# Kernel optimization log

Measured on AMD Instinct MI355X. Metric: run time of the kernel, lower is better.

Reference implementation:

```python
import jax, jax.numpy as jnp
import numpy as np

# ---- model dims (match init_kwargs) ----
BATCH, SEQ, DM = 2, 256, 768
EXPAND, HD, NST = 2, 64, 64
DI = EXPAND * DM            # 1536 d_inner
NH = DI // HD               # 24 heads
R, G = 2, 1                 # mimo_rank, ngroups
SPLIT = NST // 2            # rope_fraction=0.5 -> 32 rotated state dims
NA = SPLIT // 2             # 16 rope angles
AFLOOR, EPS = 1e-4, 1e-5
DINP = 2 * DI + 2 * NST * G * R + 3 * NH + NA  # 3416


def setup_inputs() -> dict:
    key = jax.random.key(0)
    ks = jax.random.split(key, 10)
    def n(k, shp, s=1.0):
        return jax.random.normal(k, shp, jnp.float32) * s
    u = n(ks[0], (BATCH, SEQ, DM))
    in_proj_w = n(ks[1], (DINP, DM), 0.02)
    dt_bias = n(ks[2], (NH,), 0.5)
    B_bias = jnp.ones((NH, R, NST), jnp.float32) + n(ks[3], (NH, R, NST), 0.02)
    C_bias = jnp.ones((NH, R, NST), jnp.float32) + n(ks[4], (NH, R, NST), 0.02)
    B_norm_w = jnp.ones((NST,), jnp.float32)
    C_norm_w = jnp.ones((NST,), jnp.float32)
    mimo_x = jnp.ones((NH, R, HD), jnp.float32) / R + n(ks[5], (NH, R, HD), 0.02)
    mimo_o = jnp.ones((NH, R, HD), jnp.float32) / R + n(ks[6], (NH, R, HD), 0.02)
    D = jnp.ones((NH,), jnp.float32)
    out_proj_w = n(ks[7], (DM, DI), 0.02)
    return dict(u=u, in_proj_w=in_proj_w, dt_bias=dt_bias, B_bias=B_bias,
                C_bias=C_bias, B_norm_w=B_norm_w, C_norm_w=C_norm_w,
                mimo_x=mimo_x, mimo_o=mimo_o, D=D, out_proj_w=out_proj_w)


def _rms(x, w):
    return x * jax.lax.rsqrt(jnp.mean(x * x, -1, keepdims=True) + EPS) * w


def _rope(x, theta):
    # x: (b,l,r,h,n); theta: (b,l,h,NA). Rotate first SPLIT dims in consecutive pairs.
    b, l, r, h, n = x.shape
    xr = x[..., :SPLIT].reshape(b, l, r, h, NA, 2)
    c = jnp.cos(theta)[:, :, None]            # (b,l,1,h,NA)
    s = jnp.sin(theta)[:, :, None]
    x0, x1 = xr[..., 0], xr[..., 1]
    rot = jnp.stack([x0 * c - x1 * s, x0 * s + x1 * c], -1).reshape(b, l, r, h, SPLIT)
    return jnp.concatenate([rot, x[..., SPLIT:]], -1)


def _forward(u, in_proj_w, dt_bias, B_bias, C_bias, B_norm_w, C_norm_w,
             mimo_x, mimo_o, D, out_proj_w):
    b, l, _ = u.shape
    proj = u @ in_proj_w.T                                    # (b,l,DINP)
    sp = np.cumsum([DI, DI, NST * G * R, NST * G * R, NH, NH, NH])
    z, x, Bm, Cm, dd_dt, dd_A, trap, ang = jnp.split(proj, sp, axis=-1)
    z = z.reshape(b, l, NH, HD)
    x = x.reshape(b, l, NH, HD)
    Bm = Bm.reshape(b, l, R, G, NST)[:, :, :, 0]              # g=1 -> (b,l,r,n)
    Cm = Cm.reshape(b, l, R, G, NST)[:, :, :, 0]
    A = jnp.minimum(-jax.nn.softplus(dd_A), -AFLOOR)          # (b,l,h)
    DT = jax.nn.softplus(dd_dt + dt_bias)                     # (b,l,h)
    at = jnp.exp(A * DT)                                      # decay per step
    lam = jax.nn.sigmoid(trap)                                # trapezoid blend
    Bm = _rms(Bm, B_norm_w)
    Cm = _rms(Cm, C_norm_w)
    # per-head multiplicative bias (B_bias/C_bias init to ones -> scale) : (b,l,r,h,n)
    Bh = Bm[:, :, :, None, :] * B_bias.transpose(1, 0, 2)
    Ch = Cm[:, :, :, None, :] * C_bias.transpose(1, 0, 2)
    # data-dependent rotary: cumulative angle theta_t = sum_{s<=t} dt_s * angles_s
    theta = jnp.cumsum(DT[..., None] * ang[:, :, None, :], axis=1)  # (b,l,h,NA)
    Bh = _rope(Bh, theta)
    Ch = _rope(Ch, theta)
    mv = mimo_x.transpose(1, 0, 2)                            # (r,h,p)
    mo = mimo_o.transpose(1, 0, 2)                            # (r,h,p)

    def step(carry, inp):
        S, Bp, vp = carry                                      # S:(b,r,h,p,n)
        Bt, Ct, vt, att, dtt, lamt, zt = inp
        f = jnp.einsum('brhp,brhn->brhpn', vt[:, None] * mv, Bt)
        fp = jnp.einsum('brhp,brhn->brhpn', vp[:, None] * mv, Bp)
        a5 = att[:, None, :, None, None]
        d5 = dtt[:, None, :, None, None]
        l5 = lamt[:, None, :, None, None]
        S = a5 * S + d5 * (l5 * f + (1.0 - l5) * a5 * fp)      # trapezoidal update
        y = jnp.einsum('brhn,brhpn->brhp', Ct, S)
        y = jnp.einsum('brhp,rhp->bhp', y, mo) + D[None, :, None] * vt
        y = y * jax.nn.silu(zt)                                # gated output
        return (S, Bt, vt), y

    S0 = jnp.zeros((b, R, NH, HD, NST), jnp.float32)
    B0 = jnp.zeros((b, R, NH, NST), jnp.float32)
    v0 = jnp.zeros((b, NH, HD), jnp.float32)
    inps = (jnp.moveaxis(Bh, 1, 0), jnp.moveaxis(Ch, 1, 0), jnp.moveaxis(x, 1, 0),
            jnp.moveaxis(at, 1, 0), jnp.moveaxis(DT, 1, 0), jnp.moveaxis(lam, 1, 0),
            jnp.moveaxis(z, 1, 0))
    _, ys = jax.lax.scan(step, (S0, B0, v0), inps)             # ys:(l,b,h,p)
    y = jnp.moveaxis(ys, 0, 1).reshape(b, l, DI)
    return y @ out_proj_w.T                                    # (b,l,DM)


def reference(u, in_proj_w, dt_bias, B_bias, C_bias, B_norm_w, C_norm_w,
              mimo_x, mimo_o, D, out_proj_w):
    return _forward(u, in_proj_w, dt_bias, B_bias, C_bias, B_norm_w, C_norm_w,
                    mimo_x, mimo_o, D, out_proj_w)
```

## Files before the change

### kernel.cpp

```cpp
#include <hip/hip_runtime.h>
#include <hip/hip_bf16.h>
#include <math.h>

typedef __bf16 bf16x8 __attribute__((ext_vector_type(8)));
typedef float  f32x4  __attribute__((ext_vector_type(4)));

#define BATCH 2
#define SEQ   256
#define DMODL 768
#define DIEXP 1536
#define NHEAD 24
#define HDIM  64
#define NSTATE 64
#define RRANK 2
#define NANG  16
#define HALFSPLIT 32
#define DINP  3416
#define DINP_PAD 3456
#define AFLOOR 1e-4f
#define EPSV   1e-5f

#define COL_Z    0
#define COL_X    1536
#define COL_B    3072
#define COL_C    3200
#define COL_DT   3328
#define COL_A    3352
#define COL_TRAP 3376
#define COL_ANG  3400

__device__ __forceinline__ float softplusf(float x) {
    if (x > 20.f) return x;
    return log1pf(expf(x));
}
__device__ __forceinline__ float sigmoidf_(float x) {
    return 1.f / (1.f + __expf(-x));
}
__device__ __forceinline__ ushort f2bf(float f) {
    uint u = __float_as_uint(f);
    uint r = (u + 0x7FFFu + ((u >> 16) & 1u)) >> 16;
    return (ushort)r;
}

__global__ __launch_bounds__(256) void gemm1(const float* __restrict__ A,
        const float* __restrict__ W, float* __restrict__ C, float* __restrict__ DTA) {
    const int bm = blockIdx.y * 64, bn = blockIdx.x * 64;
    const int tid = threadIdx.x;
    const int wv = tid >> 6, lane = tid & 63;
    const int wr = (wv >> 1) * 32, wc = (wv & 1) * 32;
    __shared__ ushort As[2][64 * 64];
    __shared__ ushort Bs[2][64 * 64];
    const int srow = tid >> 4, sc4 = tid & 15;
    const int NT = DMODL >> 6;
    float4 ra[4], rw[4];

    auto load_tile = [&](int t) {
        const int k0 = t * 64;
        #pragma unroll
        for (int p = 0; p < 4; ++p)
            ra[p] = *(const float4*)(A + (size_t)(bm + p * 16 + srow) * DMODL + k0 + sc4 * 4);
        #pragma unroll
        for (int p = 0; p < 4; ++p) {
            int r = p * 16 + srow;
            rw[p] = (bn + r < DINP)
                  ? *(const float4*)(W + (size_t)(bn + r) * DMODL + k0 + sc4 * 4)
                  : (float4){0.f, 0.f, 0.f, 0.f};
        }
    };
    auto write_tile = [&](int buf) {
        #pragma unroll
        for (int p = 0; p < 4; ++p) {
            int r = p * 16 + srow;
            int byt = (sc4 * 8) ^ ((r & 7) << 4);
            ushort4 h;
            h.x = f2bf(ra[p].x); h.y = f2bf(ra[p].y);
            h.z = f2bf(ra[p].z); h.w = f2bf(ra[p].w);
            *(ushort4*)(&As[buf][r * 64 + (byt >> 1)]) = h;
        }
        #pragma unroll
        for (int p = 0; p < 4; ++p) {
            int r = p * 16 + srow;
            int byt = (sc4 * 8) ^ ((r & 7) << 4);
            ushort4 h;
            h.x = f2bf(rw[p].x); h.y = f2bf(rw[p].y);
            h.z = f2bf(rw[p].z); h.w = f2bf(rw[p].w);
            *(ushort4*)(&Bs[buf][r * 64 + (byt >> 1)]) = h;
        }
    };

    f32x4 acc[2][2];
    #pragma unroll
    for (int m = 0; m < 2; ++m)
        #pragma unroll
        for (int n = 0; n < 2; ++n) acc[m][n] = (f32x4){0.f, 0.f, 0.f, 0.f};
    const int fr = lane & 15, fk = (lane >> 4) * 16;

    auto compute = [&](int buf) {
        #pragma unroll
        for (int kk = 0; kk < 2; ++kk) {
            bf16x8 af[2], bff[2];
            #pragma unroll
            for (int m = 0; m < 2; ++m) {
                int r = wr + m * 16 + fr;
                int byt = (kk * 64 + fk) ^ ((r & 7) << 4);
                af[m] = *(const bf16x8*)(&As[buf][r * 64 + (byt >> 1)]);
            }
            #pragma unroll
            for (int n = 0; n < 2; ++n) {
                int r = wc + n * 16 + fr;
                int byt = (kk * 64 + fk) ^ ((r & 7) << 4);
                bff[n] = *(const bf16x8*)(&Bs[buf][r * 64 + (byt >> 1)]);
            }
            #pragma unroll
            for (int m = 0; m < 2; ++m)
                #pragma unroll
                for (int n = 0; n < 2; ++n)
                    acc[m][n] = __builtin_amdgcn_mfma_f32_16x16x32_bf16(af[m], bff[n], acc[m][n], 0, 0, 0);
        }
    };

    load_tile(0);
    write_tile(0);
    __syncthreads();
    for (int t = 0; t < NT; ++t) {
        if (t + 1 < NT) load_tile(t + 1);
        compute(t & 1);
        if (t + 1 < NT) write_tile((t + 1) & 1);
        __syncthreads();
    }

    const int r0 = bm + wr + (lane >> 4) * 4;
    #pragma unroll
    for (int n = 0; n < 2; ++n) {
        int col = bn + wc + n * 16 + fr;
        if (col >= 3328) {
            #pragma unroll
            for (int m = 0; m < 2; ++m)
                #pragma unroll
                for (int r = 0; r < 4; ++r)
                    DTA[(size_t)(col - 3328) * 512 + r0 + m * 16 + r] = acc[m][n][r];
        }
        if (col >= DINP) continue;
        #pragma unroll
        for (int m = 0; m < 2; ++m)
            #pragma unroll
            for (int r = 0; r < 4; ++r)
                C[(size_t)(r0 + m * 16 + r) * DINP + col] = acc[m][n][r];
    }
}

__global__ __launch_bounds__(256) void gemm2(const ushort* __restrict__ A,
        const float* __restrict__ W, float* __restrict__ Part) {
    const int bm = blockIdx.y * 64, bn = blockIdx.x * 64, ks = blockIdx.z;
    const int kbase = ks * 384;
    const int tid = threadIdx.x;
    const int wv = tid >> 6, lane = tid & 63;
    const int wr = (wv >> 1) * 32, wc = (wv & 1) * 32;
    __shared__ ushort As[2][64 * 64];
    __shared__ ushort Bs[2][64 * 64];
    const int srow = tid >> 4, sc4 = tid & 15;
    const int arow = tid >> 3, acol = (tid & 7) * 8;
    const int NT = 6;
    uint4 ra[2];
    float4 rw[4];

    auto load_tile = [&](int t) {
        const int k0 = kbase + t * 64;
        #pragma unroll
        for (int p = 0; p < 2; ++p)
            ra[p] = *(const uint4*)(A + (size_t)(bm + p * 32 + arow) * DIEXP + k0 + acol);
        #pragma unroll
        for (int p = 0; p < 4; ++p)
            rw[p] = *(const float4*)(W + (size_t)(bn + p * 16 + srow) * DIEXP + k0 + sc4 * 4);
    };
    auto write_tile = [&](int buf) {
        #pragma unroll
        for (int p = 0; p < 2; ++p) {
            int r = p * 32 + arow;
            int byt = (acol * 2) ^ ((r & 7) << 4);
            *(uint4*)(&As[buf][r * 64 + (byt >> 1)]) = ra[p];
        }
        #pragma unroll
        for (int p = 0; p < 4; ++p) {
            int r = p * 16 + srow;
            int byt = (sc4 * 8) ^ ((r & 7) << 4);
            ushort4 h;
            h.x = f2bf(rw[p].x); h.y = f2bf(rw[p].y);
            h.z = f2bf(rw[p].z); h.w = f2bf(rw[p].w);
            *(ushort4*)(&Bs[buf][r * 64 + (byt >> 1)]) = h;
        }
    };

    f32x4 acc[2][2];
    #pragma unroll
    for (int m = 0; m < 2; ++m)
        #pragma unroll
        for (int n = 0; n < 2; ++n) acc[m][n] = (f32x4){0.f, 0.f, 0.f, 0.f};
    const int fr = lane & 15, fk = (lane >> 4) * 16;

    auto compute = [&](int buf) {
        #pragma unroll
        for (int kk = 0; kk < 2; ++kk) {
            bf16x8 af[2], bff[2];
            #pragma unroll
            for (int m = 0; m < 2; ++m) {
                int r = wr + m * 16 + fr;
                int byt = (kk * 64 + fk) ^ ((r & 7) << 4);
                af[m] = *(const bf16x8*)(&As[buf][r * 64 + (byt >> 1)]);
            }
            #pragma unroll
            for (int n = 0; n < 2; ++n) {
                int r = wc + n * 16 + fr;
                int byt = (kk * 64 + fk) ^ ((r & 7) << 4);
                bff[n] = *(const bf16x8*)(&Bs[buf][r * 64 + (byt >> 1)]);
            }
            #pragma unroll
            for (int m = 0; m < 2; ++m)
                #pragma unroll
                for (int n = 0; n < 2; ++n)
                    acc[m][n] = __builtin_amdgcn_mfma_f32_16x16x32_bf16(af[m], bff[n], acc[m][n], 0, 0, 0);
        }
    };

    load_tile(0);
    write_tile(0);
    __syncthreads();
    for (int t = 0; t < NT; ++t) {
        if (t + 1 < NT) load_tile(t + 1);
        compute(t & 1);
        if (t + 1 < NT) write_tile((t + 1) & 1);
        __syncthreads();
    }

    const int r0 = bm + wr + (lane >> 4) * 4;
    float* P = Part + (size_t)ks * 512 * DMODL;
    #pragma unroll
    for (int n = 0; n < 2; ++n) {
        int col = bn + wc + n * 16 + fr;
        #pragma unroll
        for (int m = 0; m < 2; ++m)
            #pragma unroll
            for (int r = 0; r < 4; ++r)
                P[(size_t)(r0 + m * 16 + r) * DMODL + col] = acc[m][n][r];
    }
}

__global__ void reduce4(const float* __restrict__ Part, float* __restrict__ out) {
    const int i = blockIdx.x * 256 + threadIdx.x;
    const float4* p4 = (const float4*)Part;
    float4 a = p4[i];
    float4 b = p4[i + 98304];
    float4 c = p4[i + 196608];
    float4 d = p4[i + 294912];
    float4 r;
    r.x = a.x + b.x + c.x + d.x;
    r.y = a.y + b.y + c.y + d.y;
    r.z = a.z + b.z + c.z + d.z;
    r.w = a.w + b.w + c.w + d.w;
    ((float4*)out)[i] = r;
}

__global__ __launch_bounds__(256) void scan_kernel(const float* __restrict__ DTA,
        const float* __restrict__ proj, const float* __restrict__ dt_bias,
        float* __restrict__ DTv, float* __restrict__ lamv, float* __restrict__ Pc,
        float* __restrict__ theta, ushort* __restrict__ XT) {
    const int bh = blockIdx.x;
    const int b = bh / NHEAD, h = bh % NHEAD;
    const int tid = threadIdx.x;
    __shared__ float mm[SEQ][18];
    __shared__ ushort tile[64][66];
    const int l = tid;
    const int gl = b * SEQ + l;
    float DT  = softplusf(DTA[(size_t)h * 512 + gl] + dt_bias[h]);
    float Asp = fmaxf(softplusf(DTA[(size_t)(24 + h) * 512 + gl]), AFLOOR);
    float la  = -Asp * DT;
    float lam = sigmoidf_(DTA[(size_t)(48 + h) * 512 + gl]);
    DTv[bh * SEQ + l] = DT;
    lamv[bh * SEQ + l] = lam;
    #pragma unroll
    for (int i = 0; i < NANG; ++i) mm[l][i] = DT * DTA[(size_t)(72 + i) * 512 + gl];
    mm[l][16] = la;
    __syncthreads();
    const int wv = tid >> 6, lane = tid & 63;
    for (int ch = wv; ch < 17; ch += 4) {
        float carry = 0.f;
        for (int seg = 0; seg < 4; ++seg) {
            float v = mm[seg * 64 + lane][ch];
            #pragma unroll
            for (int off = 1; off < 64; off <<= 1) {
                float t = __shfl_up(v, off);
                if (lane >= off) v += t;
            }
            v += carry;
            carry = __shfl(v, 63);
            int ll = seg * 64 + lane;
            if (ch < 16)
                theta[((size_t)(b * SEQ + ll) * NHEAD + h) * NANG + ch] = v;
            else
                Pc[bh * SEQ + ll] = v;
        }
    }
    for (int jt = 0; jt < 4; ++jt) {
        __syncthreads();
        for (int i = tid; i < 4096; i += 256) {
            int j = i >> 6, p = i & 63;
            tile[j][p] = f2bf(proj[(size_t)(b * SEQ + jt * 64 + j) * DINP + COL_X + h * HDIM + p]);
        }
        __syncthreads();
        for (int i = tid; i < 4096; i += 256) {
            int p = i >> 6, j = i & 63;
            XT[((size_t)bh * HDIM + p) * SEQ + jt * 64 + j] = tile[j][p];
        }
    }
}

__global__ __launch_bounds__(256) void prep3(const float* __restrict__ proj,
        const float* __restrict__ Bbias, const float* __restrict__ Cbias,
        const float* __restrict__ Bnw, const float* __restrict__ Cnw,
        const float* __restrict__ theta,
        ushort* __restrict__ Bh, ushort* __restrict__ Ch) {
    int bl = blockIdx.x;
    int b = bl / SEQ, l = bl % SEQ;
    int tid = threadIdx.x;
    __shared__ float sB[RRANK][NSTATE], sC[RRANK][NSTATE], scale[4];
    __shared__ float thl[NHEAD * NANG];
    const float* row = proj + (size_t)bl * DINP;
    if (tid < 128) {
        int r = tid / 64, n = tid % 64;
        sB[r][n] = row[COL_B + r * NSTATE + n];
    } else {
        int t2 = tid - 128;
        int r = t2 / 64, n = t2 % 64;
        sC[r][n] = row[COL_C + r * NSTATE + n];
    }
    for (int k = tid; k < NHEAD * NANG; k += 256)
        thl[k] = theta[(size_t)bl * NHEAD * NANG + k];
    __syncthreads();
    int g = tid / 64, lane = tid % 64;
    float v = (g < 2) ? sB[g][lane] : sC[g - 2][lane];
    float ss = v * v;
    #pragma unroll
    for (int off = 32; off; off >>= 1) ss += __shfl_xor(ss, off);
    if (lane == 0) scale[g] = rsqrtf(ss / NSTATE + EPSV);
    __syncthreads();
    float scB[2] = {scale[0], scale[1]};
    float scC[2] = {scale[2], scale[3]};
    for (int idx = tid; idx < RRANK * NHEAD * NSTATE; idx += 256) {
        int n = idx % NSTATE;
        int h = (idx / NSTATE) % NHEAD;
        int r = idx / (NSTATE * NHEAD);
        float outB, outC;
        if (n < HALFSPLIT) {
            int i = n >> 1;
            int n0 = i * 2, n1 = n0 + 1;
            float th = thl[h * NANG + i];
            float c = cosf(th), s = sinf(th);
            float b0 = sB[r][n0] * scB[r] * Bnw[n0] * Bbias[(h * RRANK + r) * NSTATE + n0];
            float b1 = sB[r][n1] * scB[r] * Bnw[n1] * Bbias[(h * RRANK + r) * NSTATE + n1];
            float c0 = sC[r][n0] * scC[r] * Cnw[n0] * Cbias[(h * RRANK + r) * NSTATE + n0];
            float c1 = sC[r][n1] * scC[r] * Cnw[n1] * Cbias[(h * RRANK + r) * NSTATE + n1];
            outB = (n & 1) ? (b0 * s + b1 * c) : (b0 * c - b1 * s);
            outC = (n & 1) ? (c0 * s + c1 * c) : (c0 * c - c1 * s);
        } else {
            outB = sB[r][n] * scB[r] * Bnw[n] * Bbias[(h * RRANK + r) * NSTATE + n];
            outC = sC[r][n] * scC[r] * Cnw[n] * Cbias[(h * RRANK + r) * NSTATE + n];
        }
        size_t o = ((size_t)((b * RRANK + r) * NHEAD + h) * SEQ + l) * NSTATE + n;
        Bh[o] = f2bf(outB);
        Ch[o] = f2bf(outC);
    }
}

__global__ __launch_bounds__(256) void att2(const ushort* __restrict__ Bh,
        const ushort* __restrict__ Ch, const ushort* __restrict__ XT,
        const float* __restrict__ Pc, const float* __restrict__ DTv,
        const float* __restrict__ lamv, const float* __restrict__ proj,
        const float* __restrict__ mimo_x, const float* __restrict__ mimo_o,
        const float* __restrict__ Dvec, ushort* __restrict__ Yc) {
    const int bh = blockIdx.x, tt = blockIdx.y;
    const int b = bh / NHEAD, h = bh % NHEAD;
    const int tid = threadIdx.x, wv = tid >> 6, lane = tid & 63;
    __shared__ float Pl[SEQ], u1s[SEQ], u2s[SEQ];
    __shared__ ushort Pld[2][4][16][72];
    for (int t = tid; t < SEQ; t += 256) {
        Pl[t]  = Pc[bh * SEQ + t];
        u1s[t] = DTv[bh * SEQ + t] * lamv[bh * SEQ + t];
        u2s[t] = (t + 1 < SEQ) ? DTv[bh * SEQ + t + 1] * (1.f - lamv[bh * SEQ + t + 1]) : 0.f;
    }
    __syncthreads();
    const int r16 = lane & 15, kg = (lane >> 4) * 8;
    const int trow = tt * 64 + wv * 16;
    const int tr0 = trow + (lane >> 4) * 4;
    const int brh0 = (b * RRANK + 0) * NHEAD + h;
    const int brh1 = (b * RRANK + 1) * NHEAD + h;
    bf16x8 ca[2][2];
    {
        const ushort* cp0 = Ch + ((size_t)brh0 * SEQ + trow + r16) * NSTATE + kg;
        const ushort* cp1 = Ch + ((size_t)brh1 * SEQ + trow + r16) * NSTATE + kg;
        ca[0][0] = *(const bf16x8*)cp0;  ca[0][1] = *(const bf16x8*)(cp0 + 32);
        ca[1][0] = *(const bf16x8*)cp1;  ca[1][1] = *(const bf16x8*)(cp1 + 32);
    }
    f32x4 yacc[2][4];
    #pragma unroll
    for (int r2 = 0; r2 < 2; ++r2)
        #pragma unroll
        for (int pf = 0; pf < 4; ++pf) yacc[r2][pf] = (f32x4){0.f, 0.f, 0.f, 0.f};
    float Pt[4];
    #pragma unroll
    for (int r = 0; r < 4; ++r) Pt[r] = Pl[tr0 + r];
    const float Dh = Dvec[h];

    for (int jt = 0; jt <= tt; ++jt) {
        bf16x8 xf[4][2];
        #pragma unroll
        for (int pf = 0; pf < 4; ++pf) {
            const ushort* xp = XT + ((size_t)bh * HDIM + pf * 16 + r16) * SEQ + jt * 64 + kg;
            xf[pf][0] = *(const bf16x8*)xp;
            xf[pf][1] = *(const bf16x8*)(xp + 32);
        }
        f32x4 g[2][4];
        #pragma unroll
        for (int r2 = 0; r2 < 2; ++r2) {
            const size_t bbase = (size_t)(r2 ? brh1 : brh0) * SEQ;
            #pragma unroll
            for (int nf = 0; nf < 4; ++nf) {
                const ushort* bp = Bh + (bbase + jt * 64 + nf * 16 + r16) * NSTATE + kg;
                bf16x8 b0 = *(const bf16x8*)bp;
                bf16x8 b1 = *(const bf16x8*)(bp + 32);
                f32x4 gg = (f32x4){0.f, 0.f, 0.f, 0.f};
                gg = __builtin_amdgcn_mfma_f32_16x16x32_bf16(ca[r2][0], b0, gg, 0, 0, 0);
                gg = __builtin_amdgcn_mfma_f32_16x16x32_bf16(ca[r2][1], b1, gg, 0, 0, 0);
                g[r2][nf] = gg;
            }
        }
        float w[4][4];
        #pragma unroll
        for (int nf = 0; nf < 4; ++nf) {
            const int j = jt * 64 + nf * 16 + r16;
            const float Pj = Pl[j], v1 = u1s[j], v2 = u2s[j];
            #pragma unroll
            for (int r = 0; r < 4; ++r) {
                const int t = tr0 + r;
                w[nf][r] = (j <= t) ? __expf(Pt[r] - Pj) * (v1 + ((j < t) ? v2 : 0.f)) : 0.f;
            }
        }
        #pragma unroll
        for (int r2 = 0; r2 < 2; ++r2)
            #pragma unroll
            for (int nf = 0; nf < 4; ++nf)
                #pragma unroll
                for (int r = 0; r < 4; ++r)
                    Pld[r2][wv][(lane >> 4) * 4 + r][nf * 16 + r16] = f2bf(g[r2][nf][r] * w[nf][r]);
        #pragma unroll
        for (int r2 = 0; r2 < 2; ++r2) {
            bf16x8 pa0 = *(const bf16x8*)&Pld[r2][wv][r16][kg];
            bf16x8 pa1 = *(const bf16x8*)&Pld[r2][wv][r16][32 + kg];
            #pragma unroll
            for (int pf = 0; pf < 4; ++pf) {
                yacc[r2][pf] = __builtin_amdgcn_mfma_f32_16x16x32_bf16(pa0, xf[pf][0], yacc[r2][pf], 0, 0, 0);
                yacc[r2][pf] = __builtin_amdgcn_mfma_f32_16x16x32_bf16(pa1, xf[pf][1], yacc[r2][pf], 0, 0, 0);
            }
        }
    }
    #pragma unroll
    for (int pf = 0; pf < 4; ++pf) {
        const int p = pf * 16 + r16;
        const float mm0 = mimo_x[(h * RRANK + 0) * HDIM + p] * mimo_o[(h * RRANK + 0) * HDIM + p];
        const float mm1 = mimo_x[(h * RRANK + 1) * HDIM + p] * mimo_o[(h * RRANK + 1) * HDIM + p];
        #pragma unroll
        for (int r = 0; r < 4; ++r) {
            const int t = tr0 + r;
            const float* rowp = proj + (size_t)(b * SEQ + t) * DINP;
            float xv = rowp[COL_X + h * HDIM + p];
            float zv = rowp[COL_Z + h * HDIM + p];
            float y = yacc[0][pf][r] * mm0 + yacc[1][pf][r] * mm1 + Dh * xv;
            y *= zv * sigmoidf_(zv);
            Yc[(size_t)(b * SEQ + t) * DIEXP + h * HDIM + p] = f2bf(y);
        }
    }
}

extern "C" void kernel_launch(void* const* d_in, const int* in_sizes, int n_in,
                              void* d_out, int out_size, void* d_ws, size_t ws_size,
                              hipStream_t stream) {
    const float* u        = (const float*)d_in[0];
    const float* in_w     = (const float*)d_in[1];
    const float* dt_bias  = (const float*)d_in[2];
    const float* B_bias   = (const float*)d_in[3];
    const float* C_bias   = (const float*)d_in[4];
    const float* B_norm_w = (const float*)d_in[5];
    const float* C_norm_w = (const float*)d_in[6];
    const float* mimo_x   = (const float*)d_in[7];
    const float* mimo_o   = (const float*)d_in[8];
    const float* Dvec     = (const float*)d_in[9];
    const float* out_w    = (const float*)d_in[10];
    float* out = (float*)d_out;

    float* ws = (float*)d_ws;
    float*  proj  = ws;
    float*  DTA   = proj + 1748992;
    ushort* Bh_bf = (ushort*)(DTA + 65536);
    ushort* Ch_bf = (ushort*)(DTA + 851968);
    ushort* XT_bf = (ushort*)(DTA + 1638400);
    float*  theta = DTA + 2031616;
    float*  Pc    = DTA + 2228224;
    float*  DTv   = DTA + 2240512;
    float*  lamv  = DTA + 2252800;
    ushort* Yc_bf = (ushort*)(DTA + 2265088);
    float*  Part  = DTA + 2658304;

    gemm1<<<dim3(DINP_PAD / 64, 8), 256, 0, stream>>>(u, in_w, proj, DTA);
    scan_kernel<<<BATCH * NHEAD, 256, 0, stream>>>(DTA, proj, dt_bias, DTv, lamv,
                                                   Pc, theta, XT_bf);
    prep3<<<BATCH * SEQ, 256, 0, stream>>>(proj, B_bias, C_bias, B_norm_w, C_norm_w,
                                           theta, Bh_bf, Ch_bf);
    att2<<<dim3(BATCH * NHEAD, 4), 256, 0, stream>>>(Bh_bf, Ch_bf, XT_bf, Pc, DTv,
                                                     lamv, proj, mimo_x, mimo_o,
                                                     Dvec, Yc_bf);
    gemm2<<<dim3(DMODL / 64, 8, 4), 256, 0, stream>>>(Yc_bf, out_w, Part);
    reduce4<<<384, 256, 0, stream>>>(Part, out);
}
```

Measured before the change: 76.81 us.

## Write in_proj outputs directly as bf16 head-transposed Z/X and compact B/C

The first GEMM epilogue now stages its tile in shared memory and writes Z and X as bf16 in per-head transposed layout, plus B/C as a compact bf16 array, instead of a full fp32 proj matrix. The XT transpose is dropped from the scan kernel, and prep3 and att2 read the compact bf16 buffers. This cuts global write and read traffic for the projection and removes a redundant transpose pass. In exchange the epilogue gains an extra LDS pass and barrier with 16 scalar ushort stores per thread, and Z/B/C/X values are rounded to bf16 before use.

```diff
diff --git a/kernel.cpp b/kernel.cpp
--- a/kernel.cpp
+++ b/kernel.cpp
@@ -20,15 +20,6 @@
 #define AFLOOR 1e-4f
 #define EPSV   1e-5f
 
-#define COL_Z    0
-#define COL_X    1536
-#define COL_B    3072
-#define COL_C    3200
-#define COL_DT   3328
-#define COL_A    3352
-#define COL_TRAP 3376
-#define COL_ANG  3400
-
 __device__ __forceinline__ float softplusf(float x) {
     if (x > 20.f) return x;
     return log1pf(expf(x));
@@ -41,15 +32,21 @@
     uint r = (u + 0x7FFFu + ((u >> 16) & 1u)) >> 16;
     return (ushort)r;
 }
+__device__ __forceinline__ float bf2f(ushort x) {
+    uint u = ((uint)x) << 16;
+    return __uint_as_float(u);
+}
 
 __global__ __launch_bounds__(256) void gemm1(const float* __restrict__ A,
-        const float* __restrict__ W, float* __restrict__ C, float* __restrict__ DTA) {
+        const float* __restrict__ W, ushort* __restrict__ ZT, ushort* __restrict__ XT,
+        ushort* __restrict__ BC, float* __restrict__ DTA) {
     const int bm = blockIdx.y * 64, bn = blockIdx.x * 64;
     const int tid = threadIdx.x;
     const int wv = tid >> 6, lane = tid & 63;
     const int wr = (wv >> 1) * 32, wc = (wv & 1) * 32;
     __shared__ ushort As[2][64 * 64];
     __shared__ ushort Bs[2][64 * 64];
+    __shared__ ushort Ts[64][72];
     const int srow = tid >> 4, sc4 = tid & 15;
     const int NT = DMODL >> 6;
     float4 ra[4], rw[4];
@@ -130,22 +127,42 @@
     }
 
     const int r0 = bm + wr + (lane >> 4) * 4;
-    #pragma unroll
-    for (int n = 0; n < 2; ++n) {
-        int col = bn + wc + n * 16 + fr;
-        if (col >= 3328) {
+    if (bn >= 3328) {
+        #pragma unroll
+        for (int n = 0; n < 2; ++n) {
+            int col = bn + wc + n * 16 + fr;
             #pragma unroll
             for (int m = 0; m < 2; ++m)
                 #pragma unroll
                 for (int r = 0; r < 4; ++r)
                     DTA[(size_t)(col - 3328) * 512 + r0 + m * 16 + r] = acc[m][n][r];
         }
-        if (col >= DINP) continue;
-        #pragma unroll
-        for (int m = 0; m < 2; ++m)
+        return;
+    }
+    #pragma unroll
+    for (int m = 0; m < 2; ++m)
+        #pragma unroll
+        for (int n = 0; n < 2; ++n)
             #pragma unroll
             for (int r = 0; r < 4; ++r)
-                C[(size_t)(r0 + m * 16 + r) * DINP + col] = acc[m][n][r];
+                Ts[wr + m * 16 + (lane >> 4) * 4 + r][wc + n * 16 + fr] =
+                    f2bf(acc[m][n][r]);
+    __syncthreads();
+    if (bn < 3072) {
+        const bool isX = bn >= 1536;
+        const int hh = (bn - (isX ? 1536 : 0)) >> 6;
+        const int bb = bm >> 8, l0 = bm & 255;
+        ushort* dst = (isX ? XT : ZT);
+        const int p = tid >> 2, t0 = (tid & 3) * 16;
+        ushort* o = dst + ((size_t)(bb * NHEAD + hh) * HDIM + p) * SEQ + l0 + t0;
+        #pragma unroll
+        for (int k = 0; k < 16; ++k) o[k] = Ts[t0 + k][p];
+    } else {
+        const int c0 = bn - 3072;
+        const int rr = tid >> 2, cs = (tid & 3) * 16;
+        ushort* o = BC + (size_t)(bm + rr) * 256 + c0 + cs;
+        #pragma unroll
+        for (int k = 0; k < 16; ++k) o[k] = Ts[rr][cs + k];
     }
 }
 
@@ -261,14 +278,12 @@
 }
 
 __global__ __launch_bounds__(256) void scan_kernel(const float* __restrict__ DTA,
-        const float* __restrict__ proj, const float* __restrict__ dt_bias,
-        float* __restrict__ DTv, float* __restrict__ lamv, float* __restrict__ Pc,
-        float* __restrict__ theta, ushort* __restrict__ XT) {
+        const float* __restrict__ dt_bias, float* __restrict__ DTv,
+        float* __restrict__ lamv, float* __restrict__ Pc, float* __restrict__ theta) {
     const int bh = blockIdx.x;
     const int b = bh / NHEAD, h = bh % NHEAD;
     const int tid = threadIdx.x;
     __shared__ float mm[SEQ][18];
-    __shared__ ushort tile[64][66];
     const int l = tid;
     const int gl = b * SEQ + l;
     float DT  = softplusf(DTA[(size_t)h * 512 + gl] + dt_bias[h]);
@@ -300,21 +315,9 @@
                 Pc[bh * SEQ + ll] = v;
         }
     }
-    for (int jt = 0; jt < 4; ++jt) {
-        __syncthreads();
-        for (int i = tid; i < 4096; i += 256) {
-            int j = i >> 6, p = i & 63;
-            tile[j][p] = f2bf(proj[(size_t)(b * SEQ + jt * 64 + j) * DINP + COL_X + h * HDIM + p]);
-        }
-        __syncthreads();
-        for (int i = tid; i < 4096; i += 256) {
-            int p = i >> 6, j = i & 63;
-            XT[((size_t)bh * HDIM + p) * SEQ + jt * 64 + j] = tile[j][p];
-        }
-    }
-}
-
-__global__ __launch_bounds__(256) void prep3(const float* __restrict__ proj,
+}
+
+__global__ __launch_bounds__(256) void prep3(const ushort* __restrict__ BC,
         const float* __restrict__ Bbias, const float* __restrict__ Cbias,
         const float* __restrict__ Bnw, const float* __restrict__ Cnw,
         const float* __restrict__ theta,
@@ -324,14 +327,14 @@
     int tid = threadIdx.x;
     __shared__ float sB[RRANK][NSTATE], sC[RRANK][NSTATE], scale[4];
     __shared__ float thl[NHEAD * NANG];
-    const float* row = proj + (size_t)bl * DINP;
+    const ushort* row = BC + (size_t)bl * 256;
     if (tid < 128) {
         int r = tid / 64, n = tid % 64;
-        sB[r][n] = row[COL_B + r * NSTATE + n];
+        sB[r][n] = bf2f(row[r * 64 + n]);
     } else {
         int t2 = tid - 128;
         int r = t2 / 64, n = t2 % 64;
-        sC[r][n] = row[COL_C + r * NSTATE + n];
+        sC[r][n] = bf2f(row[128 + r * 64 + n]);
     }
     for (int k = tid; k < NHEAD * NANG; k += 256)
         thl[k] = theta[(size_t)bl * NHEAD * NANG + k];
@@ -373,8 +376,8 @@
 
 __global__ __launch_bounds__(256) void att2(const ushort* __restrict__ Bh,
         const ushort* __restrict__ Ch, const ushort* __restrict__ XT,
-        const float* __restrict__ Pc, const float* __restrict__ DTv,
-        const float* __restrict__ lamv, const float* __restrict__ proj,
+        const ushort* __restrict__ ZT, const float* __restrict__ Pc,
+        const float* __restrict__ DTv, const float* __restrict__ lamv,
         const float* __restrict__ mimo_x, const float* __restrict__ mimo_o,
         const float* __restrict__ Dvec, ushort* __restrict__ Yc) {
     const int bh = blockIdx.x, tt = blockIdx.y;
@@ -467,12 +470,15 @@
         const int p = pf * 16 + r16;
         const float mm0 = mimo_x[(h * RRANK + 0) * HDIM + p] * mimo_o[(h * RRANK + 0) * HDIM + p];
         const float mm1 = mimo_x[(h * RRANK + 1) * HDIM + p] * mimo_o[(h * RRANK + 1) * HDIM + p];
+        ushort4 xv4 = *(const ushort4*)&XT[((size_t)bh * HDIM + p) * SEQ + tr0];
+        ushort4 zv4 = *(const ushort4*)&ZT[((size_t)bh * HDIM + p) * SEQ + tr0];
+        const ushort* xvp = (const ushort*)&xv4;
+        const ushort* zvp = (const ushort*)&zv4;
         #pragma unroll
         for (int r = 0; r < 4; ++r) {
             const int t = tr0 + r;
-            const float* rowp = proj + (size_t)(b * SEQ + t) * DINP;
-            float xv = rowp[COL_X + h * HDIM + p];
-            float zv = rowp[COL_Z + h * HDIM + p];
+            float xv = bf2f(xvp[r]);
+            float zv = bf2f(zvp[r]);
             float y = yacc[0][pf][r] * mm0 + yacc[1][pf][r] * mm1 + Dh * xv;
             y *= zv * sigmoidf_(zv);
             Yc[(size_t)(b * SEQ + t) * DIEXP + h * HDIM + p] = f2bf(y);
@@ -497,26 +503,25 @@
     float* out = (float*)d_out;
 
     float* ws = (float*)d_ws;
-    float*  proj  = ws;
-    float*  DTA   = proj + 1748992;
-    ushort* Bh_bf = (ushort*)(DTA + 65536);
-    ushort* Ch_bf = (ushort*)(DTA + 851968);
-    ushort* XT_bf = (ushort*)(DTA + 1638400);
-    float*  theta = DTA + 2031616;
-    float*  Pc    = DTA + 2228224;
-    float*  DTv   = DTA + 2240512;
-    float*  lamv  = DTA + 2252800;
-    ushort* Yc_bf = (ushort*)(DTA + 2265088);
-    float*  Part  = DTA + 2658304;
-
-    gemm1<<<dim3(DINP_PAD / 64, 8), 256, 0, stream>>>(u, in_w, proj, DTA);
-    scan_kernel<<<BATCH * NHEAD, 256, 0, stream>>>(DTA, proj, dt_bias, DTv, lamv,
-                                                   Pc, theta, XT_bf);
-    prep3<<<BATCH * SEQ, 256, 0, stream>>>(proj, B_bias, C_bias, B_norm_w, C_norm_w,
+    ushort* ZT    = (ushort*)(ws);
+    ushort* XT    = (ushort*)(ws + 393216);
+    ushort* BC    = (ushort*)(ws + 786432);
+    float*  DTA   = ws + 851968;
+    ushort* Bh_bf = (ushort*)(ws + 917504);
+    ushort* Ch_bf = (ushort*)(ws + 1703936);
+    float*  theta = ws + 2490368;
+    float*  Pc    = ws + 2686976;
+    float*  DTv   = ws + 2699264;
+    float*  lamv  = ws + 2711552;
+    ushort* Yc_bf = (ushort*)(ws + 2723840);
+    float*  Part  = ws + 3117056;
+
+    gemm1<<<dim3(DINP_PAD / 64, 8), 256, 0, stream>>>(u, in_w, ZT, XT, BC, DTA);
+    scan_kernel<<<BATCH * NHEAD, 256, 0, stream>>>(DTA, dt_bias, DTv, lamv, Pc, theta);
+    prep3<<<BATCH * SEQ, 256, 0, stream>>>(BC, B_bias, C_bias, B_norm_w, C_norm_w,
                                            theta, Bh_bf, Ch_bf);
-    att2<<<dim3(BATCH * NHEAD, 4), 256, 0, stream>>>(Bh_bf, Ch_bf, XT_bf, Pc, DTv,
-                                                     lamv, proj, mimo_x, mimo_o,
-                                                     Dvec, Yc_bf);
+    att2<<<dim3(BATCH * NHEAD, 4), 256, 0, stream>>>(Bh_bf, Ch_bf, XT, ZT, Pc, DTv,
+                                                     lamv, mimo_x, mimo_o, Dvec, Yc_bf);
     gemm2<<<dim3(DMODL / 64, 8, 4), 256, 0, stream>>>(Yc_bf, out_w, Part);
     reduce4<<<384, 256, 0, stream>>>(Part, out);
 }
```

Measured after the change: 66.34 us. -13.6%, faster.
